# Kernel tuning notes

Measured on AMD Instinct MI355X. Metric: run time of the kernel, lower is better.

## Reference

```python
import jax, jax.numpy as jnp
import numpy as np

# All unordered pairs of 6 ligand sites (octahedral complex)
PAIRS = np.array([(i, j) for i in range(6) for j in range(i + 1, 6)], dtype=np.int32)  # [15, 2]

B, N_LIGS, D = 32768, 6, 64
IN_DIM = D + 2 * D  # core + lig_i + lig_j = 192
H1, H2 = 64, 32


def setup_inputs() -> dict:
    key = jax.random.key(0)
    ks = jax.random.split(key, 8)
    s = 0.05  # small init scale for numerical sanity
    return {
        "core": jax.random.normal(ks[0], (B, D), dtype=jnp.float32),
        "ligs": jax.random.normal(ks[1], (B, N_LIGS, D), dtype=jnp.float32),
        "W1": jax.random.normal(ks[2], (IN_DIM, H1), dtype=jnp.float32) * s,
        "b1": jnp.zeros((H1,), dtype=jnp.float32),
        "W2": jax.random.normal(ks[3], (H1, H2), dtype=jnp.float32) * s,
        "b2": jnp.zeros((H2,), dtype=jnp.float32),
        "W3": jax.random.normal(ks[4], (H2, 1), dtype=jnp.float32) * s,
        "b3": jnp.zeros((1,), dtype=jnp.float32),
    }


def _mlp(x, W1, b1, W2, b2, W3, b3):
    # Dense(softplus) -> Dense(softplus) -> Dense(1, linear); dropout is identity at inference
    h = jax.nn.softplus(x @ W1 + b1)
    h = jax.nn.softplus(h @ W2 + b2)
    return h @ W3 + b3  # [..., 1]


def reference(core, ligs, W1, b1, W2, b2, W3, b3):
    i_idx = jnp.asarray(PAIRS[:, 0])
    j_idx = jnp.asarray(PAIRS[:, 1])
    P = PAIRS.shape[0]
    li = ligs[:, i_idx, :]  # [B, P, D]
    lj = ligs[:, j_idx, :]  # [B, P, D]
    c = jnp.broadcast_to(core[:, None, :], (core.shape[0], P, core.shape[1]))
    x1 = jnp.concatenate([c, li, lj], axis=-1)  # [B, P, 3D]
    x2 = jnp.concatenate([c, lj, li], axis=-1)  # [B, P, 3D]
    res = 0.5 * (_mlp(x1, W1, b1, W2, b2, W3, b3) + _mlp(x2, W1, b1, W2, b2, W3, b3))  # [B, P, 1]
    return jnp.sum(res, axis=1)  # [B, 1]
```

## Files before the change

### kernel.cpp

```cpp
#include <hip/hip_runtime.h>
#include <hip/hip_fp16.h>
#include <stdint.h>


typedef __attribute__((ext_vector_type(8))) _Float16 f16x8;
typedef __attribute__((ext_vector_type(2))) __fp16   fp16v2;
typedef __attribute__((ext_vector_type(4))) float    f32x4;
typedef __attribute__((ext_vector_type(4))) unsigned int u32x4;

constexpr int   BPB       = 32;
constexpr int   NT        = 1024;
constexpr int   T_STRIDE  = 1664;
constexpr int   WT_OFF    = BPB * T_STRIDE;
constexpr int   Y_OFF     = WT_OFF + 192 * 128;
constexpr int   LDS_BYTES = Y_OFF + 128;

constexpr int   WS_W1T   = 0;
constexpr int   WS_W2T   = 24576;
constexpr int   WS_B1    = 28672;
constexpr int   WS_B2    = 28928;
constexpr int   WS_W3    = 29056;

constexpr float L2E = 1.4426950408889634f;
constexpr float LN2 = 0.6931471805599453f;

constexpr unsigned long long I_BITS =
  (0ull<<0)|(0ull<<3)|(0ull<<6)|(0ull<<9)|(0ull<<12)|
  (1ull<<15)|(1ull<<18)|(1ull<<21)|(1ull<<24)|
  (2ull<<27)|(2ull<<30)|(2ull<<33)|
  (3ull<<36)|(3ull<<39)|(4ull<<42);
constexpr unsigned long long J_BITS =
  (1ull<<0)|(2ull<<3)|(3ull<<6)|(4ull<<9)|(5ull<<12)|
  (2ull<<15)|(3ull<<18)|(4ull<<21)|(5ull<<24)|
  (3ull<<27)|(4ull<<30)|(5ull<<33)|
  (4ull<<36)|(5ull<<39)|(5ull<<42);

__device__ __forceinline__ float sp2(float s) {
  float t = __builtin_amdgcn_exp2f(s);
  return __builtin_amdgcn_logf(1.0f + t);
}

__device__ __forceinline__ __half2 h1pair(__half2 u, __half2 a, __half2 b,
                                          __half2 one2) {
  __half2 s = __hadd2(__hadd2(u, a), b);
  __half2 t = h2exp2(s);
  return h2log2(__hadd2(one2, t));
}

__global__ __launch_bounds__(256)
void prep(const float* __restrict__ W1, const float* __restrict__ b1,
          const float* __restrict__ W2, const float* __restrict__ b2,
          const float* __restrict__ W3, char* __restrict__ ws)
{
  const int t = (int)(blockIdx.x * blockDim.x + threadIdx.x);
  if (t < 12288) {
    const int r = t >> 6, dl = t & 63;
    const int slab = r >> 6, n = r & 63;
    const int dg = slab * 64 + dl;
    const float v = W1[(size_t)dg * 64 + n] * L2E;
    *(uint16_t*)(ws + WS_W1T + r * 128 + (((dl >> 3) ^ (r & 7)) << 4)
                 + (dl & 7) * 2) = __half_as_ushort(__float2half(v));
  } else if (t < 14336) {
    const int e = t - 12288;
    const int k = e >> 5, m = e & 31;
    *(uint16_t*)(ws + WS_W2T + (m * 64 + k) * 2) =
        __half_as_ushort(__float2half(W2[e]));
  } else if (t < 14400) {
    ((float*)(ws + WS_B1))[t - 14336] = b1[t - 14336] * L2E;
  } else if (t < 14432) {
    ((float*)(ws + WS_B2))[t - 14400] = b2[t - 14400] * L2E;
  } else if (t < 14464) {
    ((float*)(ws + WS_W3))[t - 14432] = W3[t - 14432] * LN2;
  }
}

__global__ __launch_bounds__(NT, 8)
void tb_fused(const float* __restrict__ core, const float* __restrict__ ligs,
              const char* __restrict__ ws,   const float* __restrict__ b3,
              float* __restrict__ out)
{
  extern __shared__ char smem[];
  const int tid  = (int)threadIdx.x;
  const int lane = tid & 63;
  const int ln   = lane & 15;
  const int qd   = lane >> 4;
  const int swz  = ln & 7;
  const int wv   = __builtin_amdgcn_readfirstlane(tid >> 6);
  const int b0   = (int)blockIdx.x * BPB;

  float* yred = (float*)(smem + Y_OFF);

  const int xr = wv >> 1;
  const int mt = wv & 1;
  float4 fA[4];
  if (wv < 14) {
    const float* src = (xr == 0)
        ? (core + (size_t)(b0 + mt * 16 + ln) * 64)
        : (ligs + ((size_t)(b0 + mt * 16 + ln) * 6 + (size_t)(xr - 1)) * 64);
    #pragma unroll
    for (int ks = 0; ks < 2; ++ks) {
      fA[ks * 2 + 0] = *(const float4*)(src + ks * 32 + qd * 8);
      fA[ks * 2 + 1] = *(const float4*)(src + ks * 32 + qd * 8 + 4);
    }
  }

  {
    const uint4* src = (const uint4*)(ws + WS_W1T);
    uint4*       dst = (uint4*)(smem + WT_OFF);
    dst[tid] = src[tid];
    if (tid < 512) dst[1024 + tid] = src[1024 + tid];
  }
  if (tid < BPB) yred[tid] = 0.0f;
  __syncthreads();

  if (wv < 14) {
    union AFr { f16x8 v; fp16v2 p[4]; } Xf[2];
    #pragma unroll
    for (int ks = 0; ks < 2; ++ks) {
      Xf[ks].p[0] = __builtin_amdgcn_cvt_pkrtz(fA[ks*2].x, fA[ks*2].y);
      Xf[ks].p[1] = __builtin_amdgcn_cvt_pkrtz(fA[ks*2].z, fA[ks*2].w);
      Xf[ks].p[2] = __builtin_amdgcn_cvt_pkrtz(fA[ks*2+1].x, fA[ks*2+1].y);
      Xf[ks].p[3] = __builtin_amdgcn_cvt_pkrtz(fA[ks*2+1].z, fA[ks*2+1].w);
    }

    const int sl_lo = (xr == 0) ? 0 : 1;
    const int sl_hi = (xr == 0) ? 0 : 2;
    #pragma unroll 1
    for (int sl = sl_lo; sl <= sl_hi; ++sl) {
      const int trow = (xr == 0) ? 0 : ((sl == 1) ? xr : 6 + xr);
      #pragma unroll
      for (int nt = 0; nt < 4; ++nt) {
        f32x4 c;
        if (trow == 0) {
          c = *(const f32x4*)(ws + WS_B1 + (nt * 16 + qd * 4) * 4);
        } else {
          c = (f32x4){0.f, 0.f, 0.f, 0.f};
        }
        #pragma unroll
        for (int ks = 0; ks < 2; ++ks) {
          const f16x8 Wf = *(const f16x8*)(smem + WT_OFF
              + (sl * 64 + nt * 16 + ln) * 128 + ((((ks << 2) + qd) ^ swz) << 4));
          c = __builtin_amdgcn_mfma_f32_16x16x32_f16(Wf, Xf[ks].v, c, 0, 0, 0);
        }
        union PK { uint2 u; __half2 h[2]; } pk;
        pk.h[0] = __halves2half2(__float2half(c[0]), __float2half(c[1]));
        pk.h[1] = __halves2half2(__float2half(c[2]), __float2half(c[3]));
        *(uint2*)(smem + (size_t)(mt * 16 + ln) * T_STRIDE + trow * 128
                  + ((((nt << 1) + (qd >> 1)) ^ swz) << 4) + (qd & 1) * 8) = pk.u;
      }
    }
  }

  f16x8 W2f[2][2];
  #pragma unroll
  for (int nt = 0; nt < 2; ++nt)
    #pragma unroll
    for (int ks = 0; ks < 2; ++ks)
      W2f[nt][ks] = *(const f16x8*)(ws + WS_W2T
          + ((nt * 16 + ln) * 64 + ks * 32 + qd * 8) * 2);
  float b2v[2], w3v[2];
  #pragma unroll
  for (int nt = 0; nt < 2; ++nt) {
    b2v[nt] = ((const float*)(ws + WS_B2))[nt * 16 + ln];
    w3v[nt] = ((const float*)(ws + WS_W3))[nt * 16 + ln];
  }

  __syncthreads();

  const int mtw = wv & 1;
  const int qr  = wv >> 1;
  const __half2 one2 = __float2half2_rn(1.0f);
  const char* Tb = smem + (size_t)(mtw * 16 + ln) * T_STRIDE;
  const int k0 = ((qd)     ^ swz) << 4;
  const int k1 = ((qd + 4) ^ swz) << 4;

  union U4 { u32x4 u; __half2 h[4]; };

  U4 du0, du1;
  du0.u = *(const u32x4*)(Tb + k0);
  du1.u = *(const u32x4*)(Tb + k1);

  float yacc[4] = {0.f, 0.f, 0.f, 0.f};

  #pragma unroll 2
  for (int t3 = 0; t3 < 4; ++t3) {
    const int q = qr + 8 * t3;
    if (q >= 30) break;
    const int p  = q >> 1;
    const int iv = (int)((I_BITS >> (3 * p)) & 7ull);
    const int jv = (int)((J_BITS >> (3 * p)) & 7ull);
    const int An = (q & 1) ? jv : iv;
    const int Bn = (q & 1) ? iv : jv;
    const char* TA = Tb + (1 + An) * 128;
    const char* TB = Tb + (7 + Bn) * 128;

    U4 da0, db0, da1, db1;
    da0.u = *(const u32x4*)(TA + k0);
    db0.u = *(const u32x4*)(TB + k0);
    da1.u = *(const u32x4*)(TA + k1);
    db1.u = *(const u32x4*)(TB + k1);

    union { f16x8 v; __half2 h[4]; } A0, A1;
    #pragma unroll
    for (int w = 0; w < 4; ++w) A0.h[w] = h1pair(du0.h[w], da0.h[w], db0.h[w], one2);
    #pragma unroll
    for (int w = 0; w < 4; ++w) A1.h[w] = h1pair(du1.h[w], da1.h[w], db1.h[w], one2);

    f32x4 c0 = {b2v[0], b2v[0], b2v[0], b2v[0]};
    f32x4 c1 = {b2v[1], b2v[1], b2v[1], b2v[1]};
    c0 = __builtin_amdgcn_mfma_f32_16x16x32_f16(A0.v, W2f[0][0], c0, 0, 0, 0);
    c0 = __builtin_amdgcn_mfma_f32_16x16x32_f16(A1.v, W2f[0][1], c0, 0, 0, 0);
    c1 = __builtin_amdgcn_mfma_f32_16x16x32_f16(A0.v, W2f[1][0], c1, 0, 0, 0);
    c1 = __builtin_amdgcn_mfma_f32_16x16x32_f16(A1.v, W2f[1][1], c1, 0, 0, 0);

    #pragma unroll
    for (int reg = 0; reg < 4; ++reg) {
      yacc[reg] += sp2(c0[reg]) * w3v[0] + sp2(c1[reg]) * w3v[1];
    }
  }

  #pragma unroll
  for (int reg = 0; reg < 4; ++reg) {
    float v = yacc[reg];
    v += __shfl_xor(v, 1);
    v += __shfl_xor(v, 2);
    v += __shfl_xor(v, 4);
    v += __shfl_xor(v, 8);
    yacc[reg] = v;
  }
  if (ln == 0) {
    #pragma unroll
    for (int reg = 0; reg < 4; ++reg)
      atomicAdd(&yred[mtw * 16 + qd * 4 + reg], yacc[reg]);
  }
  __syncthreads();
  if (tid < BPB) out[b0 + tid] = 0.5f * yred[tid] + 15.0f * b3[0];
}

extern "C" void kernel_launch(void* const* d_in, const int* in_sizes, int n_in,
                              void* d_out, int out_size, void* d_ws, size_t ws_size,
                              hipStream_t stream) {
  const float* core = (const float*)d_in[0];
  const float* ligs = (const float*)d_in[1];
  const float* W1   = (const float*)d_in[2];
  const float* b1   = (const float*)d_in[3];
  const float* W2   = (const float*)d_in[4];
  const float* b2   = (const float*)d_in[5];
  const float* W3   = (const float*)d_in[6];
  const float* b3   = (const float*)d_in[7];
  float* out = (float*)d_out;
  char*  ws  = (char*)d_ws;

  const int B = in_sizes[0] / 64;
  const int grid = B / BPB;

  prep<<<dim3(57), dim3(256), 0, stream>>>(W1, b1, W2, b2, W3, ws);

  (void)hipFuncSetAttribute((const void*)tb_fused,
                            hipFuncAttributeMaxDynamicSharedMemorySize, LDS_BYTES);
  tb_fused<<<dim3(grid), dim3(NT), LDS_BYTES, stream>>>(
      core, ligs, ws, b3, out);
}
```

Baseline: 126.3 us.

## Halve block size and read W1 fragments directly from global in MFMA layout

Blocks now cover 16 batch rows with 512 threads instead of 32 rows with 1024, so each wave handles one or two of the 13 projection tiles. The prep kernel stores W1 pre-arranged in MFMA fragment order, which lets the first-layer MFMAs load weights straight from global/L2 instead of staging a 24 KB copy in LDS. This drops the LDS weight copy and the barrier after it, and shrinks LDS per block for higher occupancy. The cost is more blocks and repeated global weight reads that depend on cache hits.

```diff
diff --git a/kernel.cpp b/kernel.cpp
--- a/kernel.cpp
+++ b/kernel.cpp
@@ -8,14 +8,13 @@
 typedef __attribute__((ext_vector_type(4))) float    f32x4;
 typedef __attribute__((ext_vector_type(4))) unsigned int u32x4;
 
-constexpr int   BPB       = 32;
-constexpr int   NT        = 1024;
+constexpr int   BPB       = 16;
+constexpr int   NT        = 512;
 constexpr int   T_STRIDE  = 1664;
-constexpr int   WT_OFF    = BPB * T_STRIDE;
-constexpr int   Y_OFF     = WT_OFF + 192 * 128;
+constexpr int   Y_OFF     = BPB * T_STRIDE;
 constexpr int   LDS_BYTES = Y_OFF + 128;
 
-constexpr int   WS_W1T   = 0;
+constexpr int   WS_W1F   = 0;
 constexpr int   WS_W2T   = 24576;
 constexpr int   WS_B1    = 28672;
 constexpr int   WS_B2    = 28928;
@@ -54,12 +53,16 @@
 {
   const int t = (int)(blockIdx.x * blockDim.x + threadIdx.x);
   if (t < 12288) {
-    const int r = t >> 6, dl = t & 63;
-    const int slab = r >> 6, n = r & 63;
-    const int dg = slab * 64 + dl;
-    const float v = W1[(size_t)dg * 64 + n] * L2E;
-    *(uint16_t*)(ws + WS_W1T + r * 128 + (((dl >> 3) ^ (r & 7)) << 4)
-                 + (dl & 7) * 2) = __half_as_ushort(__float2half(v));
+    const int e  = t & 7;
+    const int ln = (t >> 3) & 15;
+    const int qd = (t >> 7) & 3;
+    const int ks = (t >> 9) & 1;
+    const int nt = (t >> 10) & 3;
+    const int sl = t >> 12;
+    const int dg = sl * 64 + ks * 32 + qd * 8 + e;
+    const int n  = nt * 16 + ln;
+    ((uint16_t*)(ws + WS_W1F))[t] =
+        __half_as_ushort(__float2half(W1[(size_t)dg * 64 + n] * L2E));
   } else if (t < 14336) {
     const int e = t - 12288;
     const int k = e >> 5, m = e & 31;
@@ -90,64 +93,70 @@
 
   float* yred = (float*)(smem + Y_OFF);
 
-  const int xr = wv >> 1;
-  const int mt = wv & 1;
-  float4 fA[4];
-  if (wv < 14) {
+  const int t1 = wv;
+  const int t2 = wv + 8;
+  const bool j2 = (wv < 5);
+
+  float4 fA[2][4];
+  {
+    const int xr = (t1 == 0) ? 0 : (t1 <= 6 ? t1 : t1 - 6);
     const float* src = (xr == 0)
-        ? (core + (size_t)(b0 + mt * 16 + ln) * 64)
-        : (ligs + ((size_t)(b0 + mt * 16 + ln) * 6 + (size_t)(xr - 1)) * 64);
+        ? (core + (size_t)(b0 + ln) * 64)
+        : (ligs + ((size_t)(b0 + ln) * 6 + (size_t)(xr - 1)) * 64);
     #pragma unroll
     for (int ks = 0; ks < 2; ++ks) {
-      fA[ks * 2 + 0] = *(const float4*)(src + ks * 32 + qd * 8);
-      fA[ks * 2 + 1] = *(const float4*)(src + ks * 32 + qd * 8 + 4);
-    }
-  }
-
-  {
-    const uint4* src = (const uint4*)(ws + WS_W1T);
-    uint4*       dst = (uint4*)(smem + WT_OFF);
-    dst[tid] = src[tid];
-    if (tid < 512) dst[1024 + tid] = src[1024 + tid];
+      fA[0][ks * 2 + 0] = *(const float4*)(src + ks * 32 + qd * 8);
+      fA[0][ks * 2 + 1] = *(const float4*)(src + ks * 32 + qd * 8 + 4);
+    }
+  }
+  if (j2) {
+    const int xr = t2 - 6;
+    const float* src = ligs + ((size_t)(b0 + ln) * 6 + (size_t)(xr - 1)) * 64;
+    #pragma unroll
+    for (int ks = 0; ks < 2; ++ks) {
+      fA[1][ks * 2 + 0] = *(const float4*)(src + ks * 32 + qd * 8);
+      fA[1][ks * 2 + 1] = *(const float4*)(src + ks * 32 + qd * 8 + 4);
+    }
   }
   if (tid < BPB) yred[tid] = 0.0f;
-  __syncthreads();
-
-  if (wv < 14) {
-    union AFr { f16x8 v; fp16v2 p[4]; } Xf[2];
+
+  union AFr { f16x8 v; fp16v2 p[4]; } Xf[2][2];
+  #pragma unroll
+  for (int jj = 0; jj < 2; ++jj) {
+    if (jj == 1 && !j2) break;
     #pragma unroll
     for (int ks = 0; ks < 2; ++ks) {
-      Xf[ks].p[0] = __builtin_amdgcn_cvt_pkrtz(fA[ks*2].x, fA[ks*2].y);
-      Xf[ks].p[1] = __builtin_amdgcn_cvt_pkrtz(fA[ks*2].z, fA[ks*2].w);
-      Xf[ks].p[2] = __builtin_amdgcn_cvt_pkrtz(fA[ks*2+1].x, fA[ks*2+1].y);
-      Xf[ks].p[3] = __builtin_amdgcn_cvt_pkrtz(fA[ks*2+1].z, fA[ks*2+1].w);
-    }
-
-    const int sl_lo = (xr == 0) ? 0 : 1;
-    const int sl_hi = (xr == 0) ? 0 : 2;
-    #pragma unroll 1
-    for (int sl = sl_lo; sl <= sl_hi; ++sl) {
-      const int trow = (xr == 0) ? 0 : ((sl == 1) ? xr : 6 + xr);
+      Xf[jj][ks].p[0] = __builtin_amdgcn_cvt_pkrtz(fA[jj][ks*2].x, fA[jj][ks*2].y);
+      Xf[jj][ks].p[1] = __builtin_amdgcn_cvt_pkrtz(fA[jj][ks*2].z, fA[jj][ks*2].w);
+      Xf[jj][ks].p[2] = __builtin_amdgcn_cvt_pkrtz(fA[jj][ks*2+1].x, fA[jj][ks*2+1].y);
+      Xf[jj][ks].p[3] = __builtin_amdgcn_cvt_pkrtz(fA[jj][ks*2+1].z, fA[jj][ks*2+1].w);
+    }
+  }
+
+  #pragma unroll
+  for (int jj = 0; jj < 2; ++jj) {
+    if (jj == 1 && !j2) break;
+    const int t  = (jj == 0) ? t1 : t2;
+    const int sl = (t == 0) ? 0 : (t <= 6 ? 1 : 2);
+    #pragma unroll
+    for (int nt = 0; nt < 4; ++nt) {
+      f32x4 c;
+      if (t == 0) {
+        c = *(const f32x4*)(ws + WS_B1 + (nt * 16 + qd * 4) * 4);
+      } else {
+        c = (f32x4){0.f, 0.f, 0.f, 0.f};
+      }
       #pragma unroll
-      for (int nt = 0; nt < 4; ++nt) {
-        f32x4 c;
-        if (trow == 0) {
-          c = *(const f32x4*)(ws + WS_B1 + (nt * 16 + qd * 4) * 4);
-        } else {
-          c = (f32x4){0.f, 0.f, 0.f, 0.f};
-        }
-        #pragma unroll
-        for (int ks = 0; ks < 2; ++ks) {
-          const f16x8 Wf = *(const f16x8*)(smem + WT_OFF
-              + (sl * 64 + nt * 16 + ln) * 128 + ((((ks << 2) + qd) ^ swz) << 4));
-          c = __builtin_amdgcn_mfma_f32_16x16x32_f16(Wf, Xf[ks].v, c, 0, 0, 0);
-        }
-        union PK { uint2 u; __half2 h[2]; } pk;
-        pk.h[0] = __halves2half2(__float2half(c[0]), __float2half(c[1]));
-        pk.h[1] = __halves2half2(__float2half(c[2]), __float2half(c[3]));
-        *(uint2*)(smem + (size_t)(mt * 16 + ln) * T_STRIDE + trow * 128
-                  + ((((nt << 1) + (qd >> 1)) ^ swz) << 4) + (qd & 1) * 8) = pk.u;
+      for (int ks = 0; ks < 2; ++ks) {
+        const f16x8 Wf = *(const f16x8*)(ws + WS_W1F
+            + (size_t)(sl * 4096 + nt * 1024 + ks * 512 + qd * 128 + ln * 8) * 2);
+        c = __builtin_amdgcn_mfma_f32_16x16x32_f16(Wf, Xf[jj][ks].v, c, 0, 0, 0);
       }
+      union PK { uint2 u; __half2 h[2]; } pk;
+      pk.h[0] = __halves2half2(__float2half(c[0]), __float2half(c[1]));
+      pk.h[1] = __halves2half2(__float2half(c[2]), __float2half(c[3]));
+      *(uint2*)(smem + (size_t)ln * T_STRIDE + t * 128
+                + ((((nt << 1) + (qd >> 1)) ^ swz) << 4) + (qd & 1) * 8) = pk.u;
     }
   }
 
@@ -167,10 +176,9 @@
 
   __syncthreads();
 
-  const int mtw = wv & 1;
-  const int qr  = wv >> 1;
+  const int qr = wv;
   const __half2 one2 = __float2half2_rn(1.0f);
-  const char* Tb = smem + (size_t)(mtw * 16 + ln) * T_STRIDE;
+  const char* Tb = smem + (size_t)ln * T_STRIDE;
   const int k0 = ((qd)     ^ swz) << 4;
   const int k1 = ((qd + 4) ^ swz) << 4;
 
@@ -231,7 +239,7 @@
   if (ln == 0) {
     #pragma unroll
     for (int reg = 0; reg < 4; ++reg)
-      atomicAdd(&yred[mtw * 16 + qd * 4 + reg], yacc[reg]);
+      atomicAdd(&yred[qd * 4 + reg], yacc[reg]);
   }
   __syncthreads();
   if (tid < BPB) out[b0 + tid] = 0.5f * yred[tid] + 15.0f * b3[0];
```

After: 128.0 us. Within noise of the previous version (+1.4%).
